# Optimization experiments

Hardware: AMD Instinct MI355X
Metric: run time of the kernel (lower is better)

## Reference

```python
import jax, jax.numpy as jnp
import numpy as np

V, D, H, F, L, M, T, B, MAXT = 32000, 1024, 16, 4096, 3, 1, 1024, 2, 2048
HD = D // H

def _ln(x, g, b, eps=1e-5):
    m = x.mean(-1, keepdims=True)
    v = ((x - m) ** 2).mean(-1, keepdims=True)
    return (x - m) * jax.lax.rsqrt(v + eps) * g + b

def _mha(x, Wq, bq, Wk, bk, Wv, bv, Wo, bo, mask):
    Bx, Tx, Dx = x.shape
    q = (x @ Wq.T + bq).reshape(Bx, Tx, H, HD)
    k = (x @ Wk.T + bk).reshape(Bx, Tx, H, HD)
    v = (x @ Wv.T + bv).reshape(Bx, Tx, H, HD)
    s = jnp.einsum('bqhd,bkhd->bhqk', q, k) / np.float32(np.sqrt(HD))
    s = jnp.where(mask[None, None], s, jnp.float32(-1e9))
    a = jax.nn.softmax(s, axis=-1)
    o = jnp.einsum('bhqk,bkhd->bqhd', a, v).reshape(Bx, Tx, Dx)
    return o @ Wo.T + bo

def setup_inputs() -> dict:
    key = jax.random.key(0)
    ks = iter(jax.random.split(key, 64))
    rn = lambda shape: jax.random.normal(next(ks), shape, jnp.float32) * 0.02
    inp = {
        'x': jax.random.randint(next(ks), (B, T), 0, V),
        'mask': jnp.tril(jnp.ones((T, T), bool)),  # causal mask
        'tok_W': rn((V, D)),  # embedding table = Linear(V,D).weight.T
        'pos_embed': rn((MAXT, D)),
        'Wq': rn((L, D, D)), 'bq': jnp.zeros((L, D)),
        'Wk': rn((L, D, D)), 'bk': jnp.zeros((L, D)),
        'Wv': rn((L, D, D)), 'bv': jnp.zeros((L, D)),
        'Wo': rn((L, D, D)), 'bo': jnp.zeros((L, D)),
        'ln1_g': jnp.ones((L, D)), 'ln1_b': jnp.zeros((L, D)),
        'W1': rn((L, F, D)), 'b1': jnp.zeros((L, F)),
        'W2': rn((L, D, F)), 'b2': jnp.zeros((L, D)),
        'ln2_g': jnp.ones((L, D)), 'ln2_b': jnp.zeros((L, D)),
        'mWq': rn((M, D, D)), 'mbq': jnp.zeros((M, D)),
        'mWk': rn((M, D, D)), 'mbk': jnp.zeros((M, D)),
        'mWv': rn((M, D, D)), 'mbv': jnp.zeros((M, D)),
        'mWo': rn((M, D, D)), 'mbo': jnp.zeros((M, D)),
        'mln_g': jnp.ones((M, D)), 'mln_b': jnp.zeros((M, D)),
        'tWq': rn((D, D)), 'tbq': jnp.zeros((D,)),
        'tWk': rn((D, D)), 'tbk': jnp.zeros((D,)),
        'tWv': rn((D, D)), 'tbv': jnp.zeros((D,)),
        'tWo': rn((D, D)), 'tbo': jnp.zeros((D,)),
        'tln_g': jnp.ones((D,)), 'tln_b': jnp.zeros((D,)),
        'norm_g': jnp.ones((D,)), 'norm_b': jnp.zeros((D,)),
        'out_W': rn((V, D)), 'out_b': jnp.zeros((V,)),
    }
    return inp

def reference(x, mask, tok_W, pos_embed, Wq, bq, Wk, bk, Wv, bv, Wo, bo,
              ln1_g, ln1_b, W1, b1, W2, b2, ln2_g, ln2_b,
              mWq, mbq, mWk, mbk, mWv, mbv, mWo, mbo, mln_g, mln_b,
              tWq, tbq, tWk, tbk, tWv, tbv, tWo, tbo, tln_g, tln_b,
              norm_g, norm_b, out_W, out_b):
    Bx, Tx = x.shape
    # one_hot(x, V).float() @ W_tok^T  ==  gather row x from the (V, D) table
    h = jnp.take(tok_W, x, axis=0) + pos_embed[:Tx][None]
    mi = 0
    for i in range(L):  # static small layer count
        a = _mha(h, Wq[i], bq[i], Wk[i], bk[i], Wv[i], bv[i], Wo[i], bo[i], mask)
        h = _ln(h + a, ln1_g[i], ln1_b[i])
        f = jax.nn.gelu(h @ W1[i].T + b1[i]) @ W2[i].T + b2[i]
        h = _ln(h + f, ln2_g[i], ln2_b[i])
        if i % 3 == 2 and mi < M:  # memory layer every 3rd block
            a = _mha(h, mWq[mi], mbq[mi], mWk[mi], mbk[mi], mWv[mi], mbv[mi], mWo[mi], mbo[mi], mask)
            h = _ln(h + a, mln_g[mi], mln_b[mi])
            mi += 1
    a = _mha(h, tWq, tbq, tWk, tbk, tWv, tbv, tWo, tbo, mask)  # thought attention
    h = _ln(h + a, tln_g, tln_b)
    h = _ln(h, norm_g, norm_b)
    return h @ out_W.T + out_b  # [B, T, V] logits
```

## Files before the change

### kernel.cpp

```cpp
#include <hip/hip_runtime.h>
#include <cstdint>

#define DEV static __device__ __forceinline__

typedef unsigned short u16;
typedef __attribute__((ext_vector_type(8))) short short8;
typedef __attribute__((ext_vector_type(4))) float f32x4;

namespace cfg {
constexpr int V = 32000, D = 1024, H = 16, F = 4096, L = 3, T = 1024, B = 2;
constexpr int N = B * T;
constexpr int HD = D / H;
}

DEV float bf2f(u16 b) { union { unsigned u; float f; } x; x.u = (unsigned)b << 16; return x.f; }
DEV u16 f2bf(float f) {
  union { float f; unsigned u; } x; x.f = f;
  unsigned u = x.u;
  return (u16)((u + 0x7fffu + ((u >> 16) & 1u)) >> 16);
}

DEV void gload16(void* lds, const void* g) {
  __builtin_amdgcn_global_load_lds((__attribute__((address_space(1))) void*)g,
                                   (__attribute__((address_space(3))) void*)lds, 16, 0, 0);
}

template <int NW>
DEV void waitVm() {
  if constexpr (NW == 0) asm volatile("s_waitcnt vmcnt(0)" ::: "memory");
  else if constexpr (NW == 4) asm volatile("s_waitcnt vmcnt(4)" ::: "memory");
  else if constexpr (NW == 8) asm volatile("s_waitcnt vmcnt(8)" ::: "memory");
  __builtin_amdgcn_sched_barrier(0);
}
DEV void barrierRaw() {
  __builtin_amdgcn_sched_barrier(0);
  __builtin_amdgcn_s_barrier();
  __builtin_amdgcn_sched_barrier(0);
}
DEV void waitLgkm0() {
  asm volatile("s_waitcnt lgkmcnt(0)" ::: "memory");
  __builtin_amdgcn_sched_barrier(0);
}

DEV float waveSum(float v) {
#pragma unroll
  for (int o = 32; o; o >>= 1) v += __shfl_xor(v, o);
  return v;
}

struct CastJob { const float* src; u16* dst; int nBlk; };
struct CastArgs { CastJob j[24]; int n; };

__global__ void cast_kernel(CastArgs a) {
  int blk = blockIdx.x;
  int i = 0;
  while (i + 1 < a.n && blk >= a.j[i].nBlk) { blk -= a.j[i].nBlk; ++i; }
  const size_t base = (size_t)blk * 2048 + threadIdx.x * 8;
  const float4* s4 = (const float4*)(a.j[i].src + base);
  const float4 v0 = s4[0], v1 = s4[1];
  short8 o;
  o[0] = (short)f2bf(v0.x); o[1] = (short)f2bf(v0.y);
  o[2] = (short)f2bf(v0.z); o[3] = (short)f2bf(v0.w);
  o[4] = (short)f2bf(v1.x); o[5] = (short)f2bf(v1.y);
  o[6] = (short)f2bf(v1.z); o[7] = (short)f2bf(v1.w);
  *(short8*)(a.j[i].dst + base) = o;
}

struct CopyJob { const float* src; float* dst; };
struct CopyArgs { CopyJob j[16]; int n; };
__global__ void bconcat_kernel(CopyArgs a) {
  const CopyJob jb = a.j[blockIdx.x];
  ((float4*)jb.dst)[threadIdx.x] = ((const float4*)jb.src)[threadIdx.x];
}

__global__ void embed_kernel(const int* __restrict__ x, const float* __restrict__ tokW,
                             const float* __restrict__ pos, float* __restrict__ hF,
                             u16* __restrict__ hB) {
  const int bt = blockIdx.x;
  const int t = bt & (cfg::T - 1);
  const int tid = threadIdx.x;
  const int idx = x[bt];
  float4 v = ((const float4*)(tokW + (size_t)idx * cfg::D))[tid];
  const float4 p = ((const float4*)(pos + (size_t)t * cfg::D))[tid];
  v.x += p.x; v.y += p.y; v.z += p.z; v.w += p.w;
  ((float4*)(hF + (size_t)bt * cfg::D))[tid] = v;
  union { u16 u[4]; uint2 q; } pk;
  pk.u[0] = f2bf(v.x); pk.u[1] = f2bf(v.y); pk.u[2] = f2bf(v.z); pk.u[3] = f2bf(v.w);
  *(uint2*)(hB + (size_t)bt * cfg::D + tid * 4) = pk.q;
}

DEV void addBf4(float4& x, const u16* p, size_t off) {
  const uint2 q = *(const uint2*)(p + off);
  x.x += bf2f((u16)(q.x & 0xffffu)); x.y += bf2f((u16)(q.x >> 16));
  x.z += bf2f((u16)(q.y & 0xffffu)); x.w += bf2f((u16)(q.y >> 16));
}

__global__ void ln4_kernel(const float* __restrict__ base,
                           const u16* __restrict__ a0, const u16* __restrict__ a1,
                           const u16* __restrict__ a2, const u16* __restrict__ a3,
                           const float* __restrict__ biasv,
                           const float* __restrict__ g, const float* __restrict__ bt,
                           float* __restrict__ outF, u16* __restrict__ outB) {
  const int row = blockIdx.x, tid = threadIdx.x;
  const int lane = tid & 63, wid = tid >> 6;
  const size_t roff = (size_t)row * cfg::D;
  const size_t eoff = roff + tid * 4;
  float4 x = ((const float4*)(base + roff))[tid];
  addBf4(x, a0, eoff); addBf4(x, a1, eoff); addBf4(x, a2, eoff); addBf4(x, a3, eoff);
  {
    const float4 a = ((const float4*)biasv)[tid];
    x.x += a.x; x.y += a.y; x.z += a.z; x.w += a.w;
  }
  float s = x.x + x.y + x.z + x.w;
  float s2 = x.x * x.x + x.y * x.y + x.z * x.z + x.w * x.w;
  __shared__ float sb[8];
  s = waveSum(s); s2 = waveSum(s2);
  if (lane == 0) { sb[wid] = s; sb[4 + wid] = s2; }
  __syncthreads();
  s = sb[0] + sb[1] + sb[2] + sb[3];
  s2 = sb[4] + sb[5] + sb[6] + sb[7];
  const float mean = s * (1.f / cfg::D);
  const float rs = rsqrtf(s2 * (1.f / cfg::D) - mean * mean + 1e-5f);
  const float4 gv = ((const float4*)g)[tid];
  const float4 bv = ((const float4*)bt)[tid];
  float4 y;
  y.x = (x.x - mean) * rs * gv.x + bv.x;
  y.y = (x.y - mean) * rs * gv.y + bv.y;
  y.z = (x.z - mean) * rs * gv.z + bv.z;
  y.w = (x.w - mean) * rs * gv.w + bv.w;
  ((float4*)(outF + roff))[tid] = y;
  union { u16 u[4]; uint2 q; } pk;
  pk.u[0] = f2bf(y.x); pk.u[1] = f2bf(y.y); pk.u[2] = f2bf(y.z); pk.u[3] = f2bf(y.w);
  *(uint2*)(outB + roff + tid * 4) = pk.q;
}

__global__ void lnfin_kernel(const float* __restrict__ base,
                             const u16* __restrict__ a0, const u16* __restrict__ a1,
                             const u16* __restrict__ a2, const u16* __restrict__ a3,
                             const float* __restrict__ biasv,
                             const float* __restrict__ g1, const float* __restrict__ b1v,
                             const float* __restrict__ g2, const float* __restrict__ b2v,
                             u16* __restrict__ outB) {
  const int row = blockIdx.x, tid = threadIdx.x;
  const int lane = tid & 63, wid = tid >> 6;
  const size_t roff = (size_t)row * cfg::D;
  const size_t eoff = roff + tid * 4;
  float4 x = ((const float4*)(base + roff))[tid];
  addBf4(x, a0, eoff); addBf4(x, a1, eoff); addBf4(x, a2, eoff); addBf4(x, a3, eoff);
  {
    const float4 a = ((const float4*)biasv)[tid];
    x.x += a.x; x.y += a.y; x.z += a.z; x.w += a.w;
  }
  __shared__ float sb[8];
  float s = x.x + x.y + x.z + x.w;
  float s2 = x.x * x.x + x.y * x.y + x.z * x.z + x.w * x.w;
  s = waveSum(s); s2 = waveSum(s2);
  if (lane == 0) { sb[wid] = s; sb[4 + wid] = s2; }
  __syncthreads();
  s = sb[0] + sb[1] + sb[2] + sb[3];
  s2 = sb[4] + sb[5] + sb[6] + sb[7];
  float mean = s * (1.f / cfg::D);
  float rs = rsqrtf(s2 * (1.f / cfg::D) - mean * mean + 1e-5f);
  const float4 g1v = ((const float4*)g1)[tid];
  const float4 b1x = ((const float4*)b1v)[tid];
  float4 y;
  y.x = (x.x - mean) * rs * g1v.x + b1x.x;
  y.y = (x.y - mean) * rs * g1v.y + b1x.y;
  y.z = (x.z - mean) * rs * g1v.z + b1x.z;
  y.w = (x.w - mean) * rs * g1v.w + b1x.w;
  float t = y.x + y.y + y.z + y.w;
  float t2 = y.x * y.x + y.y * y.y + y.z * y.z + y.w * y.w;
  t = waveSum(t); t2 = waveSum(t2);
  __syncthreads();
  if (lane == 0) { sb[wid] = t; sb[4 + wid] = t2; }
  __syncthreads();
  t = sb[0] + sb[1] + sb[2] + sb[3];
  t2 = sb[4] + sb[5] + sb[6] + sb[7];
  mean = t * (1.f / cfg::D);
  rs = rsqrtf(t2 * (1.f / cfg::D) - mean * mean + 1e-5f);
  const float4 g2v = ((const float4*)g2)[tid];
  const float4 b2x = ((const float4*)b2v)[tid];
  union { u16 u[4]; uint2 q; } pk;
  pk.u[0] = f2bf((y.x - mean) * rs * g2v.x + b2x.x);
  pk.u[1] = f2bf((y.y - mean) * rs * g2v.y + b2x.y);
  pk.u[2] = f2bf((y.z - mean) * rs * g2v.z + b2x.z);
  pk.u[3] = f2bf((y.w - mean) * rs * g2v.w + b2x.w);
  *(uint2*)(outB + roff + tid * 4) = pk.q;
}

__global__ void vtrans_kernel(const u16* __restrict__ v, u16* __restrict__ vtO, int vstride) {
  __shared__ u16 s[64][68];
  const int bh = blockIdx.y, b = bh >> 4, h = bh & 15;
  const int t0 = blockIdx.x * 64;
  const int tid = threadIdx.x;
  const int r2 = tid >> 3, cg = tid & 7;
#pragma unroll
  for (int p = 0; p < 2; ++p) {
    const int r = p * 32 + r2;
    const short8 val = *(const short8*)(v + (size_t)(b * cfg::T + t0 + r) * vstride + h * 64 + cg * 8);
#pragma unroll
    for (int j = 0; j < 8; ++j) s[r][cg * 8 + j] = (u16)val[j];
  }
  __syncthreads();
#pragma unroll
  for (int p = 0; p < 2; ++p) {
    const int d = p * 32 + r2;
    short8 o;
#pragma unroll
    for (int j = 0; j < 8; ++j) o[j] = (short)s[cg * 8 + j][d];
    *(short8*)(vtO + ((size_t)bh * 64 + d) * (size_t)cfg::T + t0 + cg * 8) = o;
  }
}

template <int NCH>
DEV void stageTile(u16* lds, const u16* src, int strideElems, int tid) {
#pragma unroll
  for (int c = 0; c < NCH / 256; ++c) {
    const int ci = c * 256 + tid;
    const int r = ci >> 3;
    const int c8 = ci & 7;
    const int sc8 = c8 ^ (r & 7);
    gload16(lds + (size_t)ci * 8, src + (size_t)r * strideElems + sc8 * 8);
  }
}
DEV short8 ldsFrag(const u16* tile, int row, int kElem) {
  const int byteoff = row * 128 + ((kElem * 2) ^ ((row & 7) << 4));
  return *(const short8*)((const char*)tile + byteoff);
}
DEV short8 ldsFrag32(const u16* tile, int row, int kElem) {
  const int byteoff = row * 64 + ((kElem * 2) ^ (((row >> 1) & 3) << 4));
  return *(const short8*)((const char*)tile + byteoff);
}

__launch_bounds__(256, 3)
__global__ void fattn_kernel(const u16* __restrict__ qkv, const u16* __restrict__ vt,
                             u16* __restrict__ o) {
  constexpr int D3 = 3 * cfg::D;
  __shared__ u16 Qs[64 * 64];
  __shared__ u16 Ks[64 * 64];
  __shared__ u16 Vs[64 * 64];
  __shared__ u16 Ps[64][72];
  const int tid = threadIdx.x, lane = tid & 63, w = tid >> 6;
  const int qt = gridDim.x - 1 - blockIdx.x;
  const int bh = blockIdx.y;
  const int b = bh >> 4, h = bh & 15;
  const int q0 = qt * 64;
  const int l15 = lane & 15, lq = lane >> 4;

  stageTile<512>(Qs, qkv + (size_t)(b * cfg::T + q0) * D3 + h * 64, D3, tid);
  __syncthreads();
  short8 qf[2];
#pragma unroll
  for (int kk = 0; kk < 2; ++kk)
    qf[kk] = ldsFrag(Qs, w * 16 + l15, kk * 32 + lq * 8);

  f32x4 oa[4];
  float m[4], l[4];
#pragma unroll
  for (int r = 0; r < 4; ++r) { m[r] = -1e30f; l[r] = 0.f; }
#pragma unroll
  for (int nt = 0; nt < 4; ++nt) { oa[nt][0] = 0; oa[nt][1] = 0; oa[nt][2] = 0; oa[nt][3] = 0; }

  const int nkt = qt + 1;
  const u16* kbase = qkv + (size_t)(b * cfg::T) * D3 + cfg::D + h * 64;
  const u16* vbase = vt + (size_t)bh * 64 * cfg::T;

  for (int kt = 0; kt < nkt; ++kt) {
    const int k0 = kt * 64;
    __syncthreads();
    stageTile<512>(Ks, kbase + (size_t)k0 * D3, D3, tid);
    stageTile<512>(Vs, vbase + k0, cfg::T, tid);
    __syncthreads();

    f32x4 sa[4];
#pragma unroll
    for (int nt = 0; nt < 4; ++nt) { sa[nt][0] = 0; sa[nt][1] = 0; sa[nt][2] = 0; sa[nt][3] = 0; }
#pragma unroll
    for (int kk = 0; kk < 2; ++kk) {
      short8 kf[4];
#pragma unroll
      for (int nt = 0; nt < 4; ++nt) kf[nt] = ldsFrag(Ks, nt * 16 + l15, kk * 32 + lq * 8);
#pragma unroll
      for (int nt = 0; nt < 4; ++nt)
        sa[nt] = __builtin_amdgcn_mfma_f32_16x16x32_bf16(qf[kk], kf[nt], sa[nt], 0, 0, 0);
    }

    const bool needMask = (kt >= qt);
#pragma unroll
    for (int r = 0; r < 4; ++r) {
      const int qrow = q0 + w * 16 + lq * 4 + r;
      float s[4];
#pragma unroll
      for (int nt = 0; nt < 4; ++nt) {
        s[nt] = sa[nt][r] * 0.125f;
        if (needMask && (k0 + nt * 16 + l15 > qrow)) s[nt] = -3e38f;
      }
      float rm = fmaxf(fmaxf(s[0], s[1]), fmaxf(s[2], s[3]));
#pragma unroll
      for (int off = 1; off < 16; off <<= 1) rm = fmaxf(rm, __shfl_xor(rm, off));
      const float mn = fmaxf(m[r], rm);
      const float sc = __expf(m[r] - mn);
      m[r] = mn;
      float ps = 0.f;
#pragma unroll
      for (int nt = 0; nt < 4; ++nt) {
        const float p = __expf(s[nt] - mn);
        ps += p;
        Ps[w * 16 + lq * 4 + r][nt * 16 + l15] = f2bf(p);
      }
#pragma unroll
      for (int off = 1; off < 16; off <<= 1) ps += __shfl_xor(ps, off);
      l[r] = l[r] * sc + ps;
#pragma unroll
      for (int nt = 0; nt < 4; ++nt) oa[nt][r] *= sc;
    }

#pragma unroll
    for (int kk = 0; kk < 2; ++kk) {
      short8 pa = *(const short8*)&Ps[w * 16 + l15][kk * 32 + lq * 8];
      short8 vf[4];
#pragma unroll
      for (int nt = 0; nt < 4; ++nt) vf[nt] = ldsFrag(Vs, nt * 16 + l15, kk * 32 + lq * 8);
#pragma unroll
      for (int nt = 0; nt < 4; ++nt)
        oa[nt] = __builtin_amdgcn_mfma_f32_16x16x32_bf16(pa, vf[nt], oa[nt], 0, 0, 0);
    }
  }

  u16* obase = o + (size_t)(b * cfg::T + q0 + w * 16) * cfg::D + h * 64;
#pragma unroll
  for (int r = 0; r < 4; ++r) {
    const float inv = 1.f / l[r];
    const int rl = lq * 4 + r;
#pragma unroll
    for (int nt = 0; nt < 4; ++nt)
      obase[(size_t)rl * cfg::D + nt * 16 + l15] = f2bf(oa[nt][r] * inv);
  }
}

template <int BN, int EPI, int OUTF32, int SWZ, int MMAJOR>
__launch_bounds__(256, 4)
__global__ void gemm_kernel(const u16* __restrict__ A, const u16* __restrict__ Bw,
                            const float* __restrict__ bias, void* __restrict__ Cp,
                            int lda, int ldb, int ldc, int K, long long partStride) {
  constexpr int BM = 128, BK = 64;
  constexpr int WN = BN / 2;
  constexpr int MF = 4, NF = WN / 16;
  int bx = blockIdx.x, by = blockIdx.y;
  if (SWZ) {
    const int gx = gridDim.x;
    const int nwg = gx * gridDim.y;
    const int lid = by * gx + bx;
    const int q = nwg >> 3, r = nwg & 7;
    const int xcd = lid & 7, rest = lid >> 3;
    const int nid = (xcd < r ? xcd * (q + 1) : r * (q + 1) + (xcd - r) * q) + rest;
    bx = nid % gx; by = nid / gx;
  }
  const int z = blockIdx.z;
  const u16* Ab = A + (size_t)z * K;
  const u16* Bb = Bw + (size_t)z * K;
  const int tid = threadIdx.x;
  const int lane = tid & 63;
  const int wid = tid >> 6;
  const int wr = wid >> 1, wc = wid & 1;
  const int m0 = (MMAJOR ? bx : by) * BM;
  const int n0 = (MMAJOR ? by : bx) * BN;

  __shared__ u16 As[BM][BK];
  __shared__ u16 Bs[BN][BK];

  const int nkt = K / BK;

  f32x4 acc[MF][NF];
#pragma unroll
  for (int i = 0; i < MF; ++i)
#pragma unroll
    for (int j = 0; j < NF; ++j) {
      acc[i][j][0] = 0.f; acc[i][j][1] = 0.f; acc[i][j][2] = 0.f; acc[i][j][3] = 0.f;
    }

  for (int kt = 0; kt < nkt; ++kt) {
    __syncthreads();
    const int kb = kt * BK;
    stageTile<(BM * BK) / 8>(&As[0][0], Ab + (size_t)m0 * lda + kb, lda, tid);
    stageTile<(BN * BK) / 8>(&Bs[0][0], Bb + (size_t)n0 * ldb + kb, ldb, tid);
    __syncthreads();
#pragma unroll
    for (int kk = 0; kk < BK / 32; ++kk) {
      short8 av[MF], bv[NF];
      const int kElem = kk * 32 + (lane >> 4) * 8;
#pragma unroll
      for (int mt = 0; mt < MF; ++mt)
        av[mt] = ldsFrag(&As[0][0], wr * 64 + mt * 16 + (lane & 15), kElem);
#pragma unroll
      for (int nt = 0; nt < NF; ++nt)
        bv[nt] = ldsFrag(&Bs[0][0], wc * WN + nt * 16 + (lane & 15), kElem);
#pragma unroll
      for (int mt = 0; mt < MF; ++mt)
#pragma unroll
        for (int nt = 0; nt < NF; ++nt)
          acc[mt][nt] = __builtin_amdgcn_mfma_f32_16x16x32_bf16(av[mt], bv[nt], acc[mt][nt], 0, 0, 0);
    }
  }

  const int rhi = (lane >> 4) * 4, cidx = lane & 15;
  const long long cb = (long long)z * partStride;
#pragma unroll
  for (int mt = 0; mt < MF; ++mt) {
#pragma unroll
    for (int nt = 0; nt < NF; ++nt) {
      const int col = n0 + wc * WN + nt * 16 + cidx;
      const float badd = bias ? bias[col] : 0.f;
#pragma unroll
      for (int r = 0; r < 4; ++r) {
        const int row = m0 + wr * 64 + mt * 16 + rhi + r;
        float val = acc[mt][nt][r] + badd;
        if (EPI == 1) {
          const float zz = 1.5957691216057308f * (val + 0.044715f * val * val * val);
          const float th = 1.f - 2.f / (__expf(zz) + 1.f);
          val = 0.5f * val * (1.f + th);
        }
        const size_t off = (size_t)(cb + (long long)row * ldc + col);
        if (OUTF32) ((float*)Cp)[off] = val;
        else ((u16*)Cp)[off] = f2bf(val);
      }
    }
  }
}

__launch_bounds__(512, 1)
__global__ void gemm256c_kernel(const u16* __restrict__ A, const u16* __restrict__ Bw,
                                const float* __restrict__ bias, float* __restrict__ Cp,
                                int lda, int ldb, int ldc, int K) {
  extern __shared__ u16 lds[];
  int bx = blockIdx.x, by = blockIdx.y;
  {
    const int gx = gridDim.x;
    const int nwg = gx * gridDim.y;
    const int lid = by * gx + bx;
    const int q = nwg >> 3, r = nwg & 7;
    const int xcd = lid & 7, rest = lid >> 3;
    const int nid = (xcd < r ? xcd * (q + 1) : r * (q + 1) + (xcd - r) * q) + rest;
    bx = nid % gx; by = nid / gx;
  }
  const int tid = threadIdx.x;
  const int lane = tid & 63;
  const int wid = tid >> 6;
  const int wr = wid >> 2, wc = wid & 3;
  const int m0 = bx * 256;
  const int n0 = by * 256;
  const int l15 = lane & 15, lq = lane >> 4;

  const u16* Abase = A + (size_t)m0 * lda;
  const u16* Bbase = Bw + (size_t)n0 * ldb;

  auto stageHalf = [&](int ldsOff, const u16* srcBase, int ld, int kb, int h) {
    const int ci = h * 512 + tid;
    const int r = ci >> 2;
    const int sc = (ci & 3) ^ ((r >> 1) & 3);
    gload16(lds + ldsOff + (size_t)ci * 8, srcBase + (size_t)r * ld + kb + sc * 8);
  };
  auto stageA = [&](int buf, int kb) {
    stageHalf(buf * 16384, Abase, lda, kb, 0);
    stageHalf(buf * 16384, Abase, lda, kb, 1);
  };
  auto stageB = [&](int buf, int kb) {
    stageHalf(buf * 16384 + 8192, Bbase, ldb, kb, 0);
    stageHalf(buf * 16384 + 8192, Bbase, ldb, kb, 1);
  };

  f32x4 acc[8][4];
#pragma unroll
  for (int i = 0; i < 8; ++i)
#pragma unroll
    for (int j = 0; j < 4; ++j) { acc[i][j][0] = 0.f; acc[i][j][1] = 0.f; acc[i][j][2] = 0.f; acc[i][j][3] = 0.f; }

  const int nt_ = K / 32;
  for (int t = 0; t < 3; ++t) { stageA(t, t * 32); stageB(t, t * 32); }

  const int kE = lq * 8;
  for (int t = 0; t < nt_; ++t) {
    if (t <= nt_ - 3) waitVm<8>();
    else if (t == nt_ - 2) waitVm<4>();
    else waitVm<0>();
    barrierRaw();
    const int buf = t & 3;
    const u16* At = lds + buf * 16384;
    const u16* Bt = lds + buf * 16384 + 8192;
    const int nbuf = (t + 3) & 3;
    const int kb3 = (t + 3) * 32;
    const bool pf = (t + 3 < nt_);
    short8 bv[4];
#pragma unroll
    for (int nt = 0; nt < 4; ++nt)
      bv[nt] = ldsFrag32(Bt, wc * 64 + nt * 16 + l15, kE);
#pragma unroll
    for (int mh = 0; mh < 2; ++mh) {
      short8 av[4];
#pragma unroll
      for (int mt = 0; mt < 4; ++mt)
        av[mt] = ldsFrag32(At, wr * 128 + mh * 64 + mt * 16 + l15, kE);
      if (pf) {
        if (mh == 0) stageA(nbuf, kb3);
        else stageB(nbuf, kb3);
      }
      waitLgkm0();
      __builtin_amdgcn_s_setprio(1);
#pragma unroll
      for (int mt = 0; mt < 4; ++mt)
#pragma unroll
        for (int nt = 0; nt < 4; ++nt)
          acc[mh * 4 + mt][nt] = __builtin_amdgcn_mfma_f32_16x16x32_bf16(av[mt], bv[nt], acc[mh * 4 + mt][nt], 0, 0, 0);
      __builtin_amdgcn_s_setprio(0);
    }
  }

#pragma unroll
  for (int g = 0; g < 8; ++g) {
#pragma unroll
    for (int nt = 0; nt < 4; ++nt) {
      const int col = n0 + wc * 64 + nt * 16 + l15;
      const float badd = bias[col];
#pragma unroll
      for (int r = 0; r < 4; ++r) {
        const int row = m0 + wr * 128 + g * 16 + lq * 4 + r;
        Cp[(size_t)row * ldc + col] = acc[g][nt][r] + badd;
      }
    }
  }
}

extern "C" void kernel_launch(void* const* d_in, const int* in_sizes, int n_in,
                              void* d_out, int out_size, void* d_ws, size_t ws_size,
                              hipStream_t stream) {
  using namespace cfg;
  (void)in_sizes; (void)n_in; (void)out_size;
  const int* x = (const int*)d_in[0];
  const float* tokW = (const float*)d_in[2];
  const float* pos = (const float*)d_in[3];
  const float* Wq = (const float*)d_in[4];  const float* bq = (const float*)d_in[5];
  const float* Wk = (const float*)d_in[6];  const float* bk = (const float*)d_in[7];
  const float* Wv = (const float*)d_in[8];  const float* bv = (const float*)d_in[9];
  const float* Wo = (const float*)d_in[10]; const float* bo = (const float*)d_in[11];
  const float* ln1g = (const float*)d_in[12]; const float* ln1b = (const float*)d_in[13];
  const float* W1 = (const float*)d_in[14]; const float* b1 = (const float*)d_in[15];
  const float* W2 = (const float*)d_in[16]; const float* b2 = (const float*)d_in[17];
  const float* ln2g = (const float*)d_in[18]; const float* ln2b = (const float*)d_in[19];
  const float* mWq = (const float*)d_in[20]; const float* mbq = (const float*)d_in[21];
  const float* mWk = (const float*)d_in[22]; const float* mbk = (const float*)d_in[23];
  const float* mWv = (const float*)d_in[24]; const float* mbv = (const float*)d_in[25];
  const float* mWo = (const float*)d_in[26]; const float* mbo = (const float*)d_in[27];
  const float* mlng = (const float*)d_in[28]; const float* mlnb = (const float*)d_in[29];
  const float* tWq = (const float*)d_in[30]; const float* tbq = (const float*)d_in[31];
  const float* tWk = (const float*)d_in[32]; const float* tbk = (const float*)d_in[33];
  const float* tWv = (const float*)d_in[34]; const float* tbv = (const float*)d_in[35];
  const float* tWo = (const float*)d_in[36]; const float* tbo = (const float*)d_in[37];
  const float* tlng = (const float*)d_in[38]; const float* tlnb = (const float*)d_in[39];
  const float* normg = (const float*)d_in[40]; const float* normb = (const float*)d_in[41];
  const float* outW = (const float*)d_in[42]; const float* outb = (const float*)d_in[43];

  const size_t DD = (size_t)D * D;
  const long long ND = (long long)N * D;
  char* wsb = (char*)d_ws;
  size_t off = 0;
  auto alloc = [&](size_t bytes) {
    void* p = wsb + off;
    off += (bytes + 255) & ~(size_t)255;
    return p;
  };
  u16* qkvW = (u16*)alloc((size_t)L * 3 * DD * 2);
  u16* mqkvW = (u16*)alloc(3 * DD * 2);
  u16* tqkvW = (u16*)alloc(3 * DD * 2);
  u16* WoB = (u16*)alloc((size_t)L * DD * 2);
  u16* W1B = (u16*)alloc((size_t)L * F * D * 2);
  u16* W2B = (u16*)alloc((size_t)L * D * F * 2);
  u16* mWoB = (u16*)alloc(DD * 2);
  u16* tWoB = (u16*)alloc(DD * 2);
  u16* outWB = (u16*)alloc((size_t)V * D * 2);
  float* biasQKV = (float*)alloc((size_t)(L + 2) * 3 * D * 4);
  float* hF = (float*)alloc((size_t)N * D * 4);
  u16* hB = (u16*)alloc((size_t)N * D * 2);
  u16* pSb = (u16*)alloc((size_t)4 * N * D * 2);
  u16* qkvB = (u16*)alloc((size_t)N * 3 * D * 2);
  u16* vtB = (u16*)alloc((size_t)N * D * 2);
  u16* oB = (u16*)alloc((size_t)N * D * 2);
  u16* f1B = (u16*)alloc((size_t)N * F * 2);
  if (off > ws_size) return;

  CastArgs ca;
  int nj = 0; long total = 0;
  auto addJob = [&](const float* s, u16* dptr, size_t n) {
    ca.j[nj].src = s; ca.j[nj].dst = dptr; ca.j[nj].nBlk = (int)(n / 2048);
    total += (long)(n / 2048); ++nj;
  };
  for (int i = 0; i < L; ++i) {
    addJob(Wq + i * DD, qkvW + (size_t)i * 3 * DD, DD);
    addJob(Wk + i * DD, qkvW + (size_t)i * 3 * DD + DD, DD);
    addJob(Wv + i * DD, qkvW + (size_t)i * 3 * DD + 2 * DD, DD);
  }
  addJob(mWq, mqkvW, DD); addJob(mWk, mqkvW + DD, DD); addJob(mWv, mqkvW + 2 * DD, DD);
  addJob(tWq, tqkvW, DD); addJob(tWk, tqkvW + DD, DD); addJob(tWv, tqkvW + 2 * DD, DD);
  addJob(Wo, WoB, (size_t)L * DD);
  addJob(W1, W1B, (size_t)L * F * D);
  addJob(W2, W2B, (size_t)L * D * F);
  addJob(mWo, mWoB, DD); addJob(tWo, tWoB, DD);
  addJob(outW, outWB, (size_t)V * D);
  ca.n = nj;
  cast_kernel<<<dim3((unsigned)total), 256, 0, stream>>>(ca);

  CopyArgs cpa;
  int nc = 0;
  auto addCopy = [&](const float* s, float* dptr) { cpa.j[nc].src = s; cpa.j[nc].dst = dptr; ++nc; };
  for (int i = 0; i < L; ++i) {
    addCopy(bq + (size_t)i * D, biasQKV + (size_t)i * 3 * D);
    addCopy(bk + (size_t)i * D, biasQKV + (size_t)i * 3 * D + D);
    addCopy(bv + (size_t)i * D, biasQKV + (size_t)i * 3 * D + 2 * D);
  }
  addCopy(mbq, biasQKV + (size_t)L * 3 * D); addCopy(mbk, biasQKV + (size_t)L * 3 * D + D);
  addCopy(mbv, biasQKV + (size_t)L * 3 * D + 2 * D);
  addCopy(tbq, biasQKV + (size_t)(L + 1) * 3 * D); addCopy(tbk, biasQKV + (size_t)(L + 1) * 3 * D + D);
  addCopy(tbv, biasQKV + (size_t)(L + 1) * 3 * D + 2 * D);
  cpa.n = nc;
  bconcat_kernel<<<dim3((unsigned)nc), 256, 0, stream>>>(cpa);

  embed_kernel<<<N, 256, 0, stream>>>(x, tokW, pos, hF, hB);

  auto mha = [&](const u16* qkvw, const float* qkvbias, const u16* wo) {
    gemm_kernel<64, 0, 0, 0, 0><<<dim3(3 * D / 64, N / 128, 1), 256, 0, stream>>>(
        hB, qkvw, qkvbias, qkvB, D, D, 3 * D, D, 0);
    vtrans_kernel<<<dim3(T / 64, B * H), 256, 0, stream>>>(qkvB + 2 * D, vtB, 3 * D);
    fattn_kernel<<<dim3(T / 64, B * H), 256, 0, stream>>>(qkvB, vtB, oB);
    gemm_kernel<64, 0, 0, 0, 0><<<dim3(D / 64, N / 128, 4), 256, 0, stream>>>(
        oB, wo, nullptr, pSb, D, D, D, 256, ND);
  };
  auto lnMha = [&](const float* obias, const float* g, const float* b_) {
    ln4_kernel<<<N, 256, 0, stream>>>(hF, pSb, pSb + ND, pSb + 2 * ND, pSb + 3 * ND,
                                      obias, g, b_, hF, hB);
  };

  int mi = 0;
  for (int i = 0; i < L; ++i) {
    mha(qkvW + (size_t)i * 3 * DD, biasQKV + (size_t)i * 3 * D, WoB + (size_t)i * DD);
    lnMha(bo + (size_t)i * D, ln1g + (size_t)i * D, ln1b + (size_t)i * D);
    gemm_kernel<64, 1, 0, 0, 0><<<dim3(F / 64, N / 128, 1), 256, 0, stream>>>(
        hB, W1B + (size_t)i * F * D, b1 + (size_t)i * F, f1B, D, D, F, D, 0);
    gemm_kernel<64, 0, 0, 0, 0><<<dim3(D / 64, N / 128, 4), 256, 0, stream>>>(
        f1B, W2B + (size_t)i * D * F, nullptr, pSb, F, F, D, 1024, ND);
    ln4_kernel<<<N, 256, 0, stream>>>(hF, pSb, pSb + ND, pSb + 2 * ND, pSb + 3 * ND,
                                      b2 + (size_t)i * D, ln2g + (size_t)i * D,
                                      ln2b + (size_t)i * D, hF, hB);
    if (i % 3 == 2 && mi < 1) {
      mha(mqkvW, biasQKV + (size_t)L * 3 * D, mWoB);
      lnMha(mbo, mlng, mlnb);
      ++mi;
    }
  }
  mha(tqkvW, biasQKV + (size_t)(L + 1) * 3 * D, tWoB);
  lnfin_kernel<<<N, 256, 0, stream>>>(hF, pSb, pSb + ND, pSb + 2 * ND, pSb + 3 * ND,
                                      tbo, tlng, tlnb, normg, normb, hB);

  hipError_t e = hipFuncSetAttribute(
      reinterpret_cast<const void*>(gemm256c_kernel),
      hipFuncAttributeMaxDynamicSharedMemorySize, 131072);
  if (e == hipSuccess) {
    gemm256c_kernel<<<dim3(N / 256, V / 256, 1), 512, 131072, stream>>>(
        hB, outWB, outb, (float*)d_out, D, D, V, D);
  } else {
    gemm_kernel<128, 0, 1, 1, 1><<<dim3(N / 128, V / 128, 1), 256, 0, stream>>>(
        hB, outWB, outb, (float*)d_out, D, D, V, D, 0);
  }
}
```

Baseline: 870.9 us.

## Read fp32 layer weights directly in GEMMs, convert to bf16 on LDS fragment load

Removes the upfront cast pass for all layer weights (QKV, Wo, W1, W2, memory and thought layers) and keeps only the output-projection cast. The layer GEMMs now stage fp32 weight tiles into LDS, using a 16-way XOR swizzle, and convert to bf16 when loading MFMA fragments. QKV reads from three separate Wq/Wk/Wv pointers chosen by row segment. This avoids a separate read-and-write of about 80M weight elements, but doubles B-tile global traffic and LDS footprint per GEMM, adds per-fragment conversion ALU, and may lower occupancy.

```diff
diff --git a/kernel.cpp b/kernel.cpp
--- a/kernel.cpp
+++ b/kernel.cpp
@@ -48,22 +48,16 @@
   return v;
 }
 
-struct CastJob { const float* src; u16* dst; int nBlk; };
-struct CastArgs { CastJob j[24]; int n; };
-
-__global__ void cast_kernel(CastArgs a) {
-  int blk = blockIdx.x;
-  int i = 0;
-  while (i + 1 < a.n && blk >= a.j[i].nBlk) { blk -= a.j[i].nBlk; ++i; }
-  const size_t base = (size_t)blk * 2048 + threadIdx.x * 8;
-  const float4* s4 = (const float4*)(a.j[i].src + base);
+__global__ void cast_kernel(const float* __restrict__ src, u16* __restrict__ dst) {
+  const size_t base = (size_t)blockIdx.x * 2048 + threadIdx.x * 8;
+  const float4* s4 = (const float4*)(src + base);
   const float4 v0 = s4[0], v1 = s4[1];
   short8 o;
   o[0] = (short)f2bf(v0.x); o[1] = (short)f2bf(v0.y);
   o[2] = (short)f2bf(v0.z); o[3] = (short)f2bf(v0.w);
   o[4] = (short)f2bf(v1.x); o[5] = (short)f2bf(v1.y);
   o[6] = (short)f2bf(v1.z); o[7] = (short)f2bf(v1.w);
-  *(short8*)(a.j[i].dst + base) = o;
+  *(short8*)(dst + base) = o;
 }
 
 struct CopyJob { const float* src; float* dst; };
@@ -231,6 +225,19 @@
   const int byteoff = row * 64 + ((kElem * 2) ^ (((row >> 1) & 3) << 4));
   return *(const short8*)((const char*)tile + byteoff);
 }
+DEV short8 ldsFragF32(const float* tile, int row, int kElem) {
+  const int k2 = kElem >> 2;
+  const int off1 = row * 256 + (((k2) ^ (row & 15)) << 4);
+  const int off2 = off1 ^ 16;
+  const f32x4 lo = *(const f32x4*)((const char*)tile + off1);
+  const f32x4 hi = *(const f32x4*)((const char*)tile + off2);
+  short8 o;
+  o[0] = (short)f2bf(lo[0]); o[1] = (short)f2bf(lo[1]);
+  o[2] = (short)f2bf(lo[2]); o[3] = (short)f2bf(lo[3]);
+  o[4] = (short)f2bf(hi[0]); o[5] = (short)f2bf(hi[1]);
+  o[6] = (short)f2bf(hi[2]); o[7] = (short)f2bf(hi[3]);
+  return o;
+}
 
 __launch_bounds__(256, 3)
 __global__ void fattn_kernel(const u16* __restrict__ qkv, const u16* __restrict__ vt,
@@ -338,9 +345,10 @@
   }
 }
 
-template <int BN, int EPI, int OUTF32, int SWZ, int MMAJOR>
+template <int BN, int EPI, int OUTF32, int SWZ, int MMAJOR, int BF32, int NSEG>
 __launch_bounds__(256, 4)
-__global__ void gemm_kernel(const u16* __restrict__ A, const u16* __restrict__ Bw,
+__global__ void gemm_kernel(const u16* __restrict__ A, const void* __restrict__ B0,
+                            const void* __restrict__ B1, const void* __restrict__ B2,
                             const float* __restrict__ bias, void* __restrict__ Cp,
                             int lda, int ldb, int ldc, int K, long long partStride) {
   constexpr int BM = 128, BK = 64;
@@ -358,7 +366,6 @@
   }
   const int z = blockIdx.z;
   const u16* Ab = A + (size_t)z * K;
-  const u16* Bb = Bw + (size_t)z * K;
   const int tid = threadIdx.x;
   const int lane = tid & 63;
   const int wid = tid >> 6;
@@ -367,7 +374,8 @@
   const int n0 = (MMAJOR ? by : bx) * BN;
 
   __shared__ u16 As[BM][BK];
-  __shared__ u16 Bs[BN][BK];
+  __shared__ u16 BsH[BF32 ? 8 : BN * BK];
+  __shared__ float BsF[BF32 ? BN * BK : 4];
 
   const int nkt = K / BK;
 
@@ -383,7 +391,35 @@
     __syncthreads();
     const int kb = kt * BK;
     stageTile<(BM * BK) / 8>(&As[0][0], Ab + (size_t)m0 * lda + kb, lda, tid);
-    stageTile<(BN * BK) / 8>(&Bs[0][0], Bb + (size_t)n0 * ldb + kb, ldb, tid);
+    if (BF32) {
+#pragma unroll
+      for (int c = 0; c < (BN * 16) / 256; ++c) {
+        const int ci = c * 256 + tid;
+        const int r = ci >> 4;
+        const int ch = ci & 15;
+        const int sc = ch ^ (r & 15);
+        const int g = n0 + r;
+        const float* basep;
+        int rr = g;
+        if (NSEG) {
+          basep = (g < 1024) ? (const float*)B0 : (g < 2048 ? (const float*)B1 : (const float*)B2);
+          rr = g & 1023;
+        } else {
+          basep = (const float*)B0;
+        }
+        gload16(&BsF[0] + (size_t)ci * 4,
+                basep + (size_t)rr * ldb + z * K + kb + sc * 4);
+      }
+    } else {
+      const u16* Bb = (const u16*)B0 + (size_t)z * K;
+#pragma unroll
+      for (int c = 0; c < (BN * BK / 8) / 256; ++c) {
+        const int ci = c * 256 + tid;
+        const int r = ci >> 3;
+        const int sc8 = (ci & 7) ^ (r & 7);
+        gload16(&BsH[0] + (size_t)ci * 8, Bb + (size_t)(n0 + r) * ldb + kb + sc8 * 8);
+      }
+    }
     __syncthreads();
 #pragma unroll
     for (int kk = 0; kk < BK / 32; ++kk) {
@@ -393,8 +429,10 @@
       for (int mt = 0; mt < MF; ++mt)
         av[mt] = ldsFrag(&As[0][0], wr * 64 + mt * 16 + (lane & 15), kElem);
 #pragma unroll
-      for (int nt = 0; nt < NF; ++nt)
-        bv[nt] = ldsFrag(&Bs[0][0], wc * WN + nt * 16 + (lane & 15), kElem);
+      for (int nt = 0; nt < NF; ++nt) {
+        const int row = wc * WN + nt * 16 + (lane & 15);
+        bv[nt] = BF32 ? ldsFragF32(&BsF[0], row, kElem) : ldsFrag(&BsH[0], row, kElem);
+      }
 #pragma unroll
       for (int mt = 0; mt < MF; ++mt)
 #pragma unroll
@@ -568,14 +606,6 @@
     off += (bytes + 255) & ~(size_t)255;
     return p;
   };
-  u16* qkvW = (u16*)alloc((size_t)L * 3 * DD * 2);
-  u16* mqkvW = (u16*)alloc(3 * DD * 2);
-  u16* tqkvW = (u16*)alloc(3 * DD * 2);
-  u16* WoB = (u16*)alloc((size_t)L * DD * 2);
-  u16* W1B = (u16*)alloc((size_t)L * F * D * 2);
-  u16* W2B = (u16*)alloc((size_t)L * D * F * 2);
-  u16* mWoB = (u16*)alloc(DD * 2);
-  u16* tWoB = (u16*)alloc(DD * 2);
   u16* outWB = (u16*)alloc((size_t)V * D * 2);
   float* biasQKV = (float*)alloc((size_t)(L + 2) * 3 * D * 4);
   float* hF = (float*)alloc((size_t)N * D * 4);
@@ -587,26 +617,7 @@
   u16* f1B = (u16*)alloc((size_t)N * F * 2);
   if (off > ws_size) return;
 
-  CastArgs ca;
-  int nj = 0; long total = 0;
-  auto addJob = [&](const float* s, u16* dptr, size_t n) {
-    ca.j[nj].src = s; ca.j[nj].dst = dptr; ca.j[nj].nBlk = (int)(n / 2048);
-    total += (long)(n / 2048); ++nj;
-  };
-  for (int i = 0; i < L; ++i) {
-    addJob(Wq + i * DD, qkvW + (size_t)i * 3 * DD, DD);
-    addJob(Wk + i * DD, qkvW + (size_t)i * 3 * DD + DD, DD);
-    addJob(Wv + i * DD, qkvW + (size_t)i * 3 * DD + 2 * DD, DD);
-  }
-  addJob(mWq, mqkvW, DD); addJob(mWk, mqkvW + DD, DD); addJob(mWv, mqkvW + 2 * DD, DD);
-  addJob(tWq, tqkvW, DD); addJob(tWk, tqkvW + DD, DD); addJob(tWv, tqkvW + 2 * DD, DD);
-  addJob(Wo, WoB, (size_t)L * DD);
-  addJob(W1, W1B, (size_t)L * F * D);
-  addJob(W2, W2B, (size_t)L * D * F);
-  addJob(mWo, mWoB, DD); addJob(tWo, tWoB, DD);
-  addJob(outW, outWB, (size_t)V * D);
-  ca.n = nj;
-  cast_kernel<<<dim3((unsigned)total), 256, 0, stream>>>(ca);
+  cast_kernel<<<dim3((unsigned)((size_t)V * D / 2048)), 256, 0, stream>>>(outW, outWB);
 
   CopyArgs cpa;
   int nc = 0;
@@ -625,13 +636,14 @@
 
   embed_kernel<<<N, 256, 0, stream>>>(x, tokW, pos, hF, hB);
 
-  auto mha = [&](const u16* qkvw, const float* qkvbias, const u16* wo) {
-    gemm_kernel<64, 0, 0, 0, 0><<<dim3(3 * D / 64, N / 128, 1), 256, 0, stream>>>(
-        hB, qkvw, qkvbias, qkvB, D, D, 3 * D, D, 0);
+  auto mha = [&](const float* wq, const float* wk, const float* wv,
+                 const float* qkvbias, const float* wo) {
+    gemm_kernel<64, 0, 0, 0, 0, 1, 1><<<dim3(3 * D / 64, N / 128, 1), 256, 0, stream>>>(
+        hB, wq, wk, wv, qkvbias, qkvB, D, D, 3 * D, D, 0);
     vtrans_kernel<<<dim3(T / 64, B * H), 256, 0, stream>>>(qkvB + 2 * D, vtB, 3 * D);
     fattn_kernel<<<dim3(T / 64, B * H), 256, 0, stream>>>(qkvB, vtB, oB);
-    gemm_kernel<64, 0, 0, 0, 0><<<dim3(D / 64, N / 128, 4), 256, 0, stream>>>(
-        oB, wo, nullptr, pSb, D, D, D, 256, ND);
+    gemm_kernel<64, 0, 0, 0, 0, 1, 0><<<dim3(D / 64, N / 128, 4), 256, 0, stream>>>(
+        oB, wo, nullptr, nullptr, nullptr, pSb, D, D, D, 256, ND);
   };
   auto lnMha = [&](const float* obias, const float* g, const float* b_) {
     ln4_kernel<<<N, 256, 0, stream>>>(hF, pSb, pSb + ND, pSb + 2 * ND, pSb + 3 * ND,
@@ -640,22 +652,22 @@
 
   int mi = 0;
   for (int i = 0; i < L; ++i) {
-    mha(qkvW + (size_t)i * 3 * DD, biasQKV + (size_t)i * 3 * D, WoB + (size_t)i * DD);
+    mha(Wq + i * DD, Wk + i * DD, Wv + i * DD, biasQKV + (size_t)i * 3 * D, Wo + i * DD);
     lnMha(bo + (size_t)i * D, ln1g + (size_t)i * D, ln1b + (size_t)i * D);
-    gemm_kernel<64, 1, 0, 0, 0><<<dim3(F / 64, N / 128, 1), 256, 0, stream>>>(
-        hB, W1B + (size_t)i * F * D, b1 + (size_t)i * F, f1B, D, D, F, D, 0);
-    gemm_kernel<64, 0, 0, 0, 0><<<dim3(D / 64, N / 128, 4), 256, 0, stream>>>(
-        f1B, W2B + (size_t)i * D * F, nullptr, pSb, F, F, D, 1024, ND);
+    gemm_kernel<64, 1, 0, 0, 0, 1, 0><<<dim3(F / 64, N / 128, 1), 256, 0, stream>>>(
+        hB, W1 + (size_t)i * F * D, nullptr, nullptr, b1 + (size_t)i * F, f1B, D, D, F, D, 0);
+    gemm_kernel<64, 0, 0, 0, 0, 1, 0><<<dim3(D / 64, N / 128, 4), 256, 0, stream>>>(
+        f1B, W2 + (size_t)i * D * F, nullptr, nullptr, nullptr, pSb, F, F, D, 1024, ND);
     ln4_kernel<<<N, 256, 0, stream>>>(hF, pSb, pSb + ND, pSb + 2 * ND, pSb + 3 * ND,
                                       b2 + (size_t)i * D, ln2g + (size_t)i * D,
                                       ln2b + (size_t)i * D, hF, hB);
     if (i % 3 == 2 && mi < 1) {
-      mha(mqkvW, biasQKV + (size_t)L * 3 * D, mWoB);
+      mha(mWq, mWk, mWv, biasQKV + (size_t)L * 3 * D, mWo);
       lnMha(mbo, mlng, mlnb);
       ++mi;
     }
   }
-  mha(tqkvW, biasQKV + (size_t)(L + 1) * 3 * D, tWoB);
+  mha(tWq, tWk, tWv, biasQKV + (size_t)(L + 1) * 3 * D, tWo);
   lnfin_kernel<<<N, 256, 0, stream>>>(hF, pSb, pSb + ND, pSb + 2 * ND, pSb + 3 * ND,
                                       tbo, tlng, tlnb, normg, normb, hB);
 
@@ -666,7 +678,7 @@
     gemm256c_kernel<<<dim3(N / 256, V / 256, 1), 512, 131072, stream>>>(
         hB, outWB, outb, (float*)d_out, D, D, V, D);
   } else {
-    gemm_kernel<128, 0, 1, 1, 1><<<dim3(N / 128, V / 128, 1), 256, 0, stream>>>(
-        hB, outWB, outb, (float*)d_out, D, D, V, D, 0);
-  }
-}
+    gemm_kernel<128, 0, 1, 1, 1, 0, 0><<<dim3(N / 128, V / 128, 1), 256, 0, stream>>>(
+        hB, outWB, nullptr, nullptr, outb, (float*)d_out, D, D, V, D, 0);
+  }
+}
```

Result: slower. 907.0 us (+4.1%).
